# Optimization experiments

Measured on AMD Instinct MI355X. Metric: run time of the kernel, lower is better.

Reference implementation:

```python
import jax, jax.numpy as jnp
import numpy as np

HIDDEN_DIM = 1024
SEQ_LEN = 4096
D_IN = 1024


def setup_inputs() -> dict:
    key = jax.random.key(0)
    ks = jax.random.split(key, 9)
    s = 1.0 / np.sqrt(D_IN)
    return {
        "q": jax.random.normal(ks[0], (SEQ_LEN, D_IN), jnp.float32),
        "k": jax.random.normal(ks[1], (SEQ_LEN, D_IN), jnp.float32),
        "v": jax.random.normal(ks[2], (SEQ_LEN, D_IN), jnp.float32),
        "Wq": jax.random.normal(ks[3], (D_IN, HIDDEN_DIM), jnp.float32) * s,
        "bq": jnp.zeros((HIDDEN_DIM,), jnp.float32),
        "Wk": jax.random.normal(ks[4], (D_IN, HIDDEN_DIM), jnp.float32) * s,
        "bk": jnp.zeros((HIDDEN_DIM,), jnp.float32),
        "Wv": jax.random.normal(ks[5], (D_IN, HIDDEN_DIM), jnp.float32) * s,
        "bv": jnpp_zeros() if False else jnp.zeros((HIDDEN_DIM,), jnp.float32),
    }


def reference(q, k, v, Wq, bq, Wk, bk, Wv, bv):
    # Dense projections (flax Dense: x @ W + b)
    query = q @ Wq + bq          # [S, H]
    key_p = k @ Wk + bk          # [S, H]
    value = v @ Wv + bv          # [S, H]
    # scores = Q K^T / sqrt(hidden_dim)  -> [S, S]
    scores = jnp.matmul(query, key_p.T) / jnp.sqrt(jnp.float32(HIDDEN_DIM))
    weights = jax.nn.softmax(scores, axis=-1)
    context = jnp.matmul(weights, value)  # [S, H]
    return context
```

## Files before the change

### kernel.cpp

```cpp
#include <hip/hip_runtime.h>


typedef short short4v __attribute__((ext_vector_type(4)));
typedef short short8  __attribute__((ext_vector_type(8)));
typedef float f32x4   __attribute__((ext_vector_type(4)));

#define MFMA16 __builtin_amdgcn_mfma_f32_16x16x32_bf16

__device__ __forceinline__ short f2bf(float f) {
    union { float f; unsigned u; } x; x.f = f;
    unsigned r = (x.u + 0x7FFFu + ((x.u >> 16) & 1u)) >> 16;
    return (short)r;
}
__device__ __forceinline__ float bf2f(short s) {
    union { unsigned u; float f; } x;
    x.u = ((unsigned)(unsigned short)s) << 16; return x.f;
}
__device__ __forceinline__ void store_out(short* p, float v) { *p = f2bf(v); }
__device__ __forceinline__ void store_out(float* p, float v) { *p = v; }

__device__ __forceinline__ void gl2lds(const short* g, short* l) {
    __builtin_amdgcn_global_load_lds(
        (const __attribute__((address_space(1))) void*)g,
        (__attribute__((address_space(3))) void*)l, 16, 0, 0);
}

__global__ __launch_bounds__(256) void prep_w(
    const float* __restrict__ W0, const float* __restrict__ W1,
    const float* __restrict__ W2, short* __restrict__ Wt)
{
    __shared__ float tile[64][65];
    const float* W = blockIdx.z == 0 ? W0 : (blockIdx.z == 1 ? W1 : W2);
    short* T = Wt + (size_t)blockIdx.z * 1048576;
    const int c0 = blockIdx.x * 64;
    const int r0 = blockIdx.y * 64;
    const int tx = threadIdx.x & 63;
    const int ty = threadIdx.x >> 6;
    #pragma unroll
    for (int p = 0; p < 16; ++p) {
        int r = ty + p * 4;
        tile[r][tx] = W[(size_t)(r0 + r) * 1024 + c0 + tx];
    }
    __syncthreads();
    #pragma unroll
    for (int p = 0; p < 16; ++p) {
        int r = ty + p * 4;
        T[(size_t)(c0 + r) * 1024 + r0 + tx] = f2bf(tile[tx][r]);
    }
}

__global__ __launch_bounds__(256) void cast_qkv(
    const float* __restrict__ q, const float* __restrict__ k,
    const float* __restrict__ v, short* __restrict__ xb)
{
    const float* src = blockIdx.z == 0 ? q : (blockIdx.z == 1 ? k : v);
    short* dst = xb + (size_t)blockIdx.z * 4194304;
    for (int i = blockIdx.x * 256 + threadIdx.x; i < 1048576; i += 256 * 1024) {
        float4 f = ((const float4*)src)[i];
        short4v o;
        o[0] = f2bf(f.x); o[1] = f2bf(f.y); o[2] = f2bf(f.z); o[3] = f2bf(f.w);
        ((short4v*)dst)[i] = o;
    }
}

template <typename TOut, int MODE>
__global__ __launch_bounds__(256) void gemm64(
    const short* __restrict__ A, const short* __restrict__ Bt,
    const float* __restrict__ b0, const float* __restrict__ b1,
    const float* __restrict__ b2, TOut* __restrict__ C,
    short* __restrict__ Vt,
    int M, int N, int Kd, int lda, int ldb, float scale, int kiters)
{
    constexpr int LDSN = (MODE == 1) ? (128 * 136) : (128 * 64 * 2);
    __shared__ short Lds[LDSN];
    short* As = Lds;
    short* Bs = Lds + 128 * 64;

    const int t    = threadIdx.x;
    const int lane = t & 63;
    const int wv   = t >> 6;

    const int nb  = gridDim.x;
    const int bid = blockIdx.y * nb + blockIdx.x;
    const int band   = bid / (8 * nb);
    const int within = bid - band * 8 * nb;
    const int m0 = (band * 8 + (within & 7)) * 128;
    const int n0 = (within >> 3) * 128;

    const float* bias = nullptr;
    int kbeg = 0;
    if constexpr (MODE == 1) {
        const int z = blockIdx.z;
        A  += (size_t)z * M * lda;
        Bt += (size_t)z * N * ldb;
        C  += (size_t)z * M * N;
        bias = z == 0 ? b0 : (z == 1 ? b1 : b2);
    }
    if constexpr (MODE == 2) {
        kbeg = blockIdx.z * kiters * 64;
        C += (size_t)blockIdx.z * M * N;
    }
    (void)b0; (void)b1; (void)b2;

    const int sr = lane >> 3;
    const int sc = (lane & 7) ^ sr;
    const short* pA = A  + (size_t)(m0 + wv * 32 + sr) * lda + kbeg + sc * 8;
    const short* pB = Bt + (size_t)(n0 + wv * 32 + sr) * ldb + kbeg + sc * 8;
    const size_t a8 = (size_t)8 * lda;
    const size_t b8 = (size_t)8 * ldb;
    short* lA = As + wv * 2048;
    short* lB = Bs + wv * 2048;

    const int wm = wv & 1, wn = wv >> 1;
    const int lr = lane & 15, lq = lane >> 4;
    const int xkey = lr & 7;

    f32x4 acc[4][4];
    #pragma unroll
    for (int i = 0; i < 4; ++i)
        #pragma unroll
        for (int j = 0; j < 4; ++j) {
            f32x4 z = {0.f, 0.f, 0.f, 0.f};
            acc[i][j] = z;
        }

    for (int kk = 0; kk < kiters; ++kk) {
        #pragma unroll
        for (int r = 0; r < 4; ++r) gl2lds(pA + r * a8, lA + r * 512);
        #pragma unroll
        for (int r = 0; r < 4; ++r) gl2lds(pB + r * b8, lB + r * 512);
        pA += 64; pB += 64;
        __syncthreads();

        #pragma unroll
        for (int h = 0; h < 2; ++h) {
            short8 af[4], bfr[4];
            #pragma unroll
            for (int i = 0; i < 4; ++i)
                af[i] = *(const short8*)
                    &As[(wm * 64 + i * 16 + lr) * 64 + (((h * 4 + lq) ^ xkey) * 8)];
            #pragma unroll
            for (int j = 0; j < 4; ++j)
                bfr[j] = *(const short8*)
                    &Bs[(wn * 64 + j * 16 + lr) * 64 + (((h * 4 + lq) ^ xkey) * 8)];
            #pragma unroll
            for (int i = 0; i < 4; ++i)
                #pragma unroll
                for (int j = 0; j < 4; ++j)
                    acc[i][j] = MFMA16(af[i], bfr[j], acc[i][j], 0, 0, 0);
        }
        __syncthreads();
    }

    if constexpr (MODE == 1) {
        if (blockIdx.z == 2) {
            #pragma unroll
            for (int i = 0; i < 4; ++i) {
                #pragma unroll
                for (int j = 0; j < 4; ++j) {
                    const int colL = wn * 64 + j * 16 + lr;
                    const float bb = bias[n0 + colL];
                    #pragma unroll
                    for (int r = 0; r < 4; ++r) {
                        const int rowL = wm * 64 + i * 16 + lq * 4 + r;
                        Lds[colL * 136 + rowL] = f2bf(acc[i][j][r] * scale + bb);
                    }
                }
            }
            __syncthreads();
            const int c = t >> 1, part = t & 1;
            short* dst = Vt + (size_t)(n0 + c) * 4096 + m0 + part * 64;
            #pragma unroll
            for (int s = 0; s < 8; ++s)
                *(short8*)(dst + s * 8) =
                    *(const short8*)&Lds[c * 136 + part * 64 + s * 8];
            return;
        }
    }
    #pragma unroll
    for (int i = 0; i < 4; ++i) {
        #pragma unroll
        for (int j = 0; j < 4; ++j) {
            const int crow = m0 + wm * 64 + i * 16 + lq * 4;
            const int ccol = n0 + wn * 64 + j * 16 + lr;
            float bb = 0.f;
            if constexpr (MODE == 1) bb = bias[ccol];
            #pragma unroll
            for (int r = 0; r < 4; ++r) {
                float val = acc[i][j][r] * scale + bb;
                store_out(&C[(size_t)(crow + r) * N + ccol], val);
            }
        }
    }
}

__global__ __launch_bounds__(256) void softmax_bf16(short* __restrict__ S)
{
    const int row = blockIdx.x;
    short8* r8 = (short8*)(S + (size_t)row * 4096);
    const int t = threadIdx.x;

    float x[16];
    #pragma unroll
    for (int i = 0; i < 2; ++i) {
        short8 raw = r8[t + 256 * i];
        #pragma unroll
        for (int j = 0; j < 8; ++j) x[8 * i + j] = bf2f(raw[j]);
    }
    float m = -1e30f;
    #pragma unroll
    for (int i = 0; i < 16; ++i) m = fmaxf(m, x[i]);
    #pragma unroll
    for (int off = 32; off > 0; off >>= 1) m = fmaxf(m, __shfl_xor(m, off));

    __shared__ float redm[4], reds[4];
    const int wv = t >> 6;
    if ((t & 63) == 0) redm[wv] = m;
    __syncthreads();
    m = fmaxf(fmaxf(redm[0], redm[1]), fmaxf(redm[2], redm[3]));

    float s = 0.f;
    #pragma unroll
    for (int i = 0; i < 16; ++i) { x[i] = __expf(x[i] - m); s += x[i]; }
    #pragma unroll
    for (int off = 32; off > 0; off >>= 1) s += __shfl_xor(s, off);
    if ((t & 63) == 0) reds[wv] = s;
    __syncthreads();
    s = reds[0] + reds[1] + reds[2] + reds[3];
    const float inv = 1.f / s;

    #pragma unroll
    for (int i = 0; i < 2; ++i) {
        short8 o;
        #pragma unroll
        for (int j = 0; j < 8; ++j) o[j] = f2bf(x[8 * i + j] * inv);
        r8[t + 256 * i] = o;
    }
}

__global__ __launch_bounds__(256) void combine(
    const float* __restrict__ p0, const float* __restrict__ p1,
    float* __restrict__ out)
{
    for (int i = blockIdx.x * 256 + threadIdx.x; i < 1048576; i += 256 * 1024) {
        float4 a = ((const float4*)p0)[i];
        float4 b = ((const float4*)p1)[i];
        float4 o; o.x = a.x + b.x; o.y = a.y + b.y;
        o.z = a.z + b.z; o.w = a.w + b.w;
        ((float4*)out)[i] = o;
    }
}

extern "C" void kernel_launch(void* const* d_in, const int* in_sizes, int n_in,
                              void* d_out, int out_size, void* d_ws, size_t ws_size,
                              hipStream_t stream)
{
    const float* q  = (const float*)d_in[0];
    const float* k  = (const float*)d_in[1];
    const float* v  = (const float*)d_in[2];
    const float* Wq = (const float*)d_in[3];
    const float* bq = (const float*)d_in[4];
    const float* Wk = (const float*)d_in[5];
    const float* bk = (const float*)d_in[6];
    const float* Wv = (const float*)d_in[7];
    const float* bv = (const float*)d_in[8];
    float* out = (float*)d_out;

    char* ws = (char*)d_ws;
    const size_t MB = 1ull << 20;
    short* Wt = (short*)(ws + 0);
    short* xb = (short*)(ws + 6 * MB);
    short* pr = (short*)(ws + 30 * MB);
    short* Vt = (short*)(ws + 46 * MB);
    short* S  = (short*)(ws + 54 * MB);
    float* p0 = (float*)(ws + 0);
    float* p1 = p0 + 4194304;

    prep_w<<<dim3(16, 16, 3), 256, 0, stream>>>(Wq, Wk, Wv, Wt);
    cast_qkv<<<dim3(1024, 1, 3), 256, 0, stream>>>(q, k, v, xb);
    gemm64<short, 1><<<dim3(8, 32, 3), 256, 0, stream>>>(
        xb, Wt, bq, bk, bv, pr, Vt, 4096, 1024, 1024, 1024, 1024, 1.f, 16);
    gemm64<short, 0><<<dim3(32, 32), 256, 0, stream>>>(
        pr, pr + 4194304, nullptr, nullptr, nullptr, S, nullptr,
        4096, 4096, 1024, 1024, 1024, 0.03125f, 16);
    softmax_bf16<<<4096, 256, 0, stream>>>(S);
    gemm64<float, 2><<<dim3(8, 32, 2), 256, 0, stream>>>(
        S, Vt, nullptr, nullptr, nullptr, p0, nullptr,
        4096, 1024, 4096, 4096, 4096, 1.f, 32);
    combine<<<1024, 256, 0, stream>>>(p0, p1, out);
}
```

Before: 269.4 us.

## Replace 128x128 GEMM with 256x256 tile, 4-stage pipelined LDS GEMM and split-K

Replaces the 128x128, 256-thread GEMM kernel with a 256x256, 512-thread kernel. It runs a 4-deep global-to-LDS prefetch ring with explicit vmcnt waits and barriers, and raises wave priority around the MFMA blocks. The V transpose moves out of the projection epilogue into a separate transpose kernel. The final P·V GEMM uses 3- or 4-way split-K, chosen by workspace size, and the partials are summed in a generalized combine. The aim is more data reuse per tile and hiding global load latency behind MFMA work. In exchange, fewer blocks are launched, register pressure rises, and an extra transpose pass is added.

```diff
diff --git a/kernel.cpp b/kernel.cpp
--- a/kernel.cpp
+++ b/kernel.cpp
@@ -63,132 +63,153 @@
     }
 }
 
+__global__ __launch_bounds__(256) void transpose_v(
+    const short* __restrict__ src, short* __restrict__ dst)
+{
+    __shared__ short t[64][65];
+    const int c0 = blockIdx.x * 64;
+    const int r0 = blockIdx.y * 64;
+    const int tx = threadIdx.x & 63;
+    const int ty = threadIdx.x >> 6;
+    #pragma unroll
+    for (int p = 0; p < 16; ++p) {
+        const int r = p * 4 + ty;
+        t[r][tx] = src[(size_t)(r0 + r) * 1024 + c0 + tx];
+    }
+    __syncthreads();
+    #pragma unroll
+    for (int p = 0; p < 16; ++p) {
+        const int r = p * 4 + ty;
+        dst[(size_t)(c0 + r) * 4096 + r0 + tx] = t[tx][r];
+    }
+}
+
 template <typename TOut, int MODE>
-__global__ __launch_bounds__(256) void gemm64(
+__global__ __launch_bounds__(512, 2) void gemm256(
     const short* __restrict__ A, const short* __restrict__ Bt,
     const float* __restrict__ b0, const float* __restrict__ b1,
-    const float* __restrict__ b2, TOut* __restrict__ C,
-    short* __restrict__ Vt,
-    int M, int N, int Kd, int lda, int ldb, float scale, int kiters)
-{
-    constexpr int LDSN = (MODE == 1) ? (128 * 136) : (128 * 64 * 2);
-    __shared__ short Lds[LDSN];
-    short* As = Lds;
-    short* Bs = Lds + 128 * 64;
+    const float* __restrict__ b2,
+    TOut* __restrict__ C, float* __restrict__ P1, float* __restrict__ P2,
+    float* __restrict__ P3,
+    int M, int N, int lda, int ldb, float scale,
+    int nc, int nc_last, int kstep)
+{
+    __shared__ short Lds[65536];
 
     const int t    = threadIdx.x;
     const int lane = t & 63;
     const int wv   = t >> 6;
 
-    const int nb  = gridDim.x;
-    const int bid = blockIdx.y * nb + blockIdx.x;
-    const int band   = bid / (8 * nb);
-    const int within = bid - band * 8 * nb;
-    const int m0 = (band * 8 + (within & 7)) * 128;
-    const int n0 = (within >> 3) * 128;
+    int m0, n0;
+    {
+        const int nb  = gridDim.x;
+        const int bid = blockIdx.y * nb + blockIdx.x;
+        if (nb == 16 && gridDim.y == 16) {
+            const int x = bid & 7, i = bid >> 3;
+            m0 = ((x & 1) * 8 + (i & 7)) * 256;
+            n0 = ((x >> 1) * 4 + (i >> 3)) * 256;
+        } else {
+            const int band   = bid / (8 * nb);
+            const int within = bid - band * 8 * nb;
+            m0 = (band * 8 + (within & 7)) * 256;
+            n0 = (within >> 3) * 256;
+        }
+    }
 
     const float* bias = nullptr;
     int kbeg = 0;
+    TOut* Cw = C;
     if constexpr (MODE == 1) {
         const int z = blockIdx.z;
         A  += (size_t)z * M * lda;
         Bt += (size_t)z * N * ldb;
-        C  += (size_t)z * M * N;
+        Cw  = C + (size_t)z * M * N;
         bias = z == 0 ? b0 : (z == 1 ? b1 : b2);
     }
     if constexpr (MODE == 2) {
-        kbeg = blockIdx.z * kiters * 64;
-        C += (size_t)blockIdx.z * M * N;
-    }
-    (void)b0; (void)b1; (void)b2;
-
-    const int sr = lane >> 3;
-    const int sc = (lane & 7) ^ sr;
-    const short* pA = A  + (size_t)(m0 + wv * 32 + sr) * lda + kbeg + sc * 8;
-    const short* pB = Bt + (size_t)(n0 + wv * 32 + sr) * ldb + kbeg + sc * 8;
-    const size_t a8 = (size_t)8 * lda;
-    const size_t b8 = (size_t)8 * ldb;
-    short* lA = As + wv * 2048;
-    short* lB = Bs + wv * 2048;
-
-    const int wm = wv & 1, wn = wv >> 1;
+        const int z = blockIdx.z;
+        kbeg = z * kstep;
+        if (z == (int)gridDim.z - 1) nc = nc_last;
+        Cw = (TOut*)(z == 0 ? (float*)C : (z == 1 ? P1 : (z == 2 ? P2 : P3)));
+    }
+    (void)b0; (void)b1; (void)b2; (void)P1; (void)P2; (void)P3;
+    (void)nc_last; (void)kstep;
+
+    const int srow = lane >> 2;
+    const int skof = (lane & 3) * 8;
+    const short* pA0 = A  + (size_t)(m0 + wv * 16 + srow) * lda + kbeg + skof;
+    const short* pA1 = pA0 + (size_t)128 * lda;
+    const short* pB0 = Bt + (size_t)(n0 + wv * 16 + srow) * ldb + kbeg + skof;
+    const short* pB1 = pB0 + (size_t)128 * ldb;
+    short* sA0 = Lds + wv * 512;
+    short* sA1 = Lds + 4096  + wv * 512;
+    short* sB0 = Lds + 8192  + wv * 512;
+    short* sB1 = Lds + 12288 + wv * 512;
+
+    const int wm = wv >> 2, wn = wv & 3;
     const int lr = lane & 15, lq = lane >> 4;
-    const int xkey = lr & 7;
-
-    f32x4 acc[4][4];
-    #pragma unroll
-    for (int i = 0; i < 4; ++i)
+    const short* rdA = Lds + (wm * 128 + lr) * 32 + lq * 8;
+    const short* rdB = Lds + 8192 + (wn * 64 + lr) * 32 + lq * 8;
+
+    f32x4 acc[8][4];
+    #pragma unroll
+    for (int i = 0; i < 8; ++i)
+        #pragma unroll
+        for (int j = 0; j < 4; ++j) { f32x4 z4 = {0.f,0.f,0.f,0.f}; acc[i][j] = z4; }
+
+#define STAGE(c) {                                                        \
+    const int su_ = (c) & 3;                                              \
+    const size_t ko_ = (size_t)(c) * 32;                                  \
+    gl2lds(pA0 + ko_, sA0 + su_ * 16384);                                 \
+    gl2lds(pA1 + ko_, sA1 + su_ * 16384);                                 \
+    gl2lds(pB0 + ko_, sB0 + su_ * 16384);                                 \
+    gl2lds(pB1 + ko_, sB1 + su_ * 16384); }
+
+    STAGE(0); STAGE(1); STAGE(2);
+    asm volatile("s_waitcnt vmcnt(8)" ::: "memory");
+    __builtin_amdgcn_s_barrier();
+
+#define PHASE(c, DOSTAGE, VMN) {                                          \
+    const int u_ = (c) & 3;                                               \
+    const short* rA_ = rdA + u_ * 16384;                                  \
+    const short* rB_ = rdB + u_ * 16384;                                  \
+    short8 af[8], bfr[4];                                                 \
+    _Pragma("unroll") for (int i = 0; i < 8; ++i)                         \
+        af[i] = *(const short8*)(rA_ + i * 512);                          \
+    _Pragma("unroll") for (int j = 0; j < 4; ++j)                         \
+        bfr[j] = *(const short8*)(rB_ + j * 512);                         \
+    if (DOSTAGE) STAGE((c) + 3);                                          \
+    __builtin_amdgcn_s_barrier();                                         \
+    __builtin_amdgcn_s_setprio(1);                                        \
+    _Pragma("unroll") for (int i = 0; i < 8; ++i)                         \
+        _Pragma("unroll") for (int j = 0; j < 4; ++j)                     \
+            acc[i][j] = MFMA16(af[i], bfr[j], acc[i][j], 0, 0, 0);        \
+    __builtin_amdgcn_s_setprio(0);                                        \
+    if ((VMN) == 8)      asm volatile("s_waitcnt vmcnt(8)" ::: "memory"); \
+    else if ((VMN) == 4) asm volatile("s_waitcnt vmcnt(4)" ::: "memory"); \
+    else if ((VMN) == 0) asm volatile("s_waitcnt vmcnt(0)" ::: "memory"); \
+    if ((VMN) >= 0) __builtin_amdgcn_s_barrier(); }
+
+    #pragma unroll 4
+    for (int c = 0; c < nc - 3; ++c) PHASE(c, 1, 8);
+    PHASE(nc - 3, 0, 4);
+    PHASE(nc - 2, 0, 0);
+    PHASE(nc - 1, 0, -1);
+#undef PHASE
+#undef STAGE
+
+    #pragma unroll
+    for (int i = 0; i < 8; ++i) {
+        const int crow = m0 + wm * 128 + i * 16 + lq * 4;
         #pragma unroll
         for (int j = 0; j < 4; ++j) {
-            f32x4 z = {0.f, 0.f, 0.f, 0.f};
-            acc[i][j] = z;
-        }
-
-    for (int kk = 0; kk < kiters; ++kk) {
-        #pragma unroll
-        for (int r = 0; r < 4; ++r) gl2lds(pA + r * a8, lA + r * 512);
-        #pragma unroll
-        for (int r = 0; r < 4; ++r) gl2lds(pB + r * b8, lB + r * 512);
-        pA += 64; pB += 64;
-        __syncthreads();
-
-        #pragma unroll
-        for (int h = 0; h < 2; ++h) {
-            short8 af[4], bfr[4];
-            #pragma unroll
-            for (int i = 0; i < 4; ++i)
-                af[i] = *(const short8*)
-                    &As[(wm * 64 + i * 16 + lr) * 64 + (((h * 4 + lq) ^ xkey) * 8)];
-            #pragma unroll
-            for (int j = 0; j < 4; ++j)
-                bfr[j] = *(const short8*)
-                    &Bs[(wn * 64 + j * 16 + lr) * 64 + (((h * 4 + lq) ^ xkey) * 8)];
-            #pragma unroll
-            for (int i = 0; i < 4; ++i)
-                #pragma unroll
-                for (int j = 0; j < 4; ++j)
-                    acc[i][j] = MFMA16(af[i], bfr[j], acc[i][j], 0, 0, 0);
-        }
-        __syncthreads();
-    }
-
-    if constexpr (MODE == 1) {
-        if (blockIdx.z == 2) {
-            #pragma unroll
-            for (int i = 0; i < 4; ++i) {
-                #pragma unroll
-                for (int j = 0; j < 4; ++j) {
-                    const int colL = wn * 64 + j * 16 + lr;
-                    const float bb = bias[n0 + colL];
-                    #pragma unroll
-                    for (int r = 0; r < 4; ++r) {
-                        const int rowL = wm * 64 + i * 16 + lq * 4 + r;
-                        Lds[colL * 136 + rowL] = f2bf(acc[i][j][r] * scale + bb);
-                    }
-                }
-            }
-            __syncthreads();
-            const int c = t >> 1, part = t & 1;
-            short* dst = Vt + (size_t)(n0 + c) * 4096 + m0 + part * 64;
-            #pragma unroll
-            for (int s = 0; s < 8; ++s)
-                *(short8*)(dst + s * 8) =
-                    *(const short8*)&Lds[c * 136 + part * 64 + s * 8];
-            return;
-        }
-    }
-    #pragma unroll
-    for (int i = 0; i < 4; ++i) {
-        #pragma unroll
-        for (int j = 0; j < 4; ++j) {
-            const int crow = m0 + wm * 64 + i * 16 + lq * 4;
             const int ccol = n0 + wn * 64 + j * 16 + lr;
             float bb = 0.f;
             if constexpr (MODE == 1) bb = bias[ccol];
             #pragma unroll
             for (int r = 0; r < 4; ++r) {
                 float val = acc[i][j][r] * scale + bb;
-                store_out(&C[(size_t)(crow + r) * N + ccol], val);
+                store_out(&Cw[(size_t)(crow + r) * N + ccol], val);
             }
         }
     }
@@ -239,14 +260,19 @@
 }
 
 __global__ __launch_bounds__(256) void combine(
-    const float* __restrict__ p0, const float* __restrict__ p1,
-    float* __restrict__ out)
+    float* __restrict__ out, const float* __restrict__ a,
+    const float* __restrict__ b, const float* __restrict__ c, int np)
 {
     for (int i = blockIdx.x * 256 + threadIdx.x; i < 1048576; i += 256 * 1024) {
-        float4 a = ((const float4*)p0)[i];
-        float4 b = ((const float4*)p1)[i];
-        float4 o; o.x = a.x + b.x; o.y = a.y + b.y;
-        o.z = a.z + b.z; o.w = a.w + b.w;
+        float4 o = ((const float4*)out)[i];
+        float4 x = ((const float4*)a)[i];
+        float4 y = ((const float4*)b)[i];
+        o.x += x.x + y.x; o.y += x.y + y.y;
+        o.z += x.z + y.z; o.w += x.w + y.w;
+        if (np == 3) {
+            float4 w = ((const float4*)c)[i];
+            o.x += w.x; o.y += w.y; o.z += w.z; o.w += w.w;
+        }
         ((float4*)out)[i] = o;
     }
 }
@@ -271,21 +297,33 @@
     short* Wt = (short*)(ws + 0);
     short* xb = (short*)(ws + 6 * MB);
     short* pr = (short*)(ws + 30 * MB);
-    short* Vt = (short*)(ws + 46 * MB);
-    short* S  = (short*)(ws + 54 * MB);
-    float* p0 = (float*)(ws + 0);
-    float* p1 = p0 + 4194304;
+    short* S  = (short*)(ws + 46 * MB);
+    short* Vt = (short*)(ws + 78 * MB);
+    float* p1 = (float*)(ws + 0);
+    float* p2 = (float*)(ws + 16 * MB);
+    float* p3 = (float*)(ws + 86 * MB);
+    const int SK = (ws_size >= 102 * MB) ? 4 : 3;
 
     prep_w<<<dim3(16, 16, 3), 256, 0, stream>>>(Wq, Wk, Wv, Wt);
     cast_qkv<<<dim3(1024, 1, 3), 256, 0, stream>>>(q, k, v, xb);
-    gemm64<short, 1><<<dim3(8, 32, 3), 256, 0, stream>>>(
-        xb, Wt, bq, bk, bv, pr, Vt, 4096, 1024, 1024, 1024, 1024, 1.f, 16);
-    gemm64<short, 0><<<dim3(32, 32), 256, 0, stream>>>(
-        pr, pr + 4194304, nullptr, nullptr, nullptr, S, nullptr,
-        4096, 4096, 1024, 1024, 1024, 0.03125f, 16);
+    gemm256<short, 1><<<dim3(4, 16, 3), 512, 0, stream>>>(
+        xb, Wt, bq, bk, bv, pr, nullptr, nullptr, nullptr,
+        4096, 1024, 1024, 1024, 1.f, 32, 32, 0);
+    transpose_v<<<dim3(16, 64), 256, 0, stream>>>(pr + 8 * 1024 * 1024, Vt);
+    gemm256<short, 0><<<dim3(16, 16), 512, 0, stream>>>(
+        pr, pr + 4 * 1024 * 1024, nullptr, nullptr, nullptr, S,
+        nullptr, nullptr, nullptr,
+        4096, 4096, 1024, 1024, 0.03125f, 32, 32, 0);
     softmax_bf16<<<4096, 256, 0, stream>>>(S);
-    gemm64<float, 2><<<dim3(8, 32, 2), 256, 0, stream>>>(
-        S, Vt, nullptr, nullptr, nullptr, p0, nullptr,
-        4096, 1024, 4096, 4096, 4096, 1.f, 32);
-    combine<<<1024, 256, 0, stream>>>(p0, p1, out);
-}
+    if (SK == 4) {
+        gemm256<float, 2><<<dim3(4, 16, 4), 512, 0, stream>>>(
+            S, Vt, nullptr, nullptr, nullptr, out, p1, p2, p3,
+            4096, 1024, 4096, 4096, 1.f, 32, 32, 1024);
+        combine<<<1024, 256, 0, stream>>>(out, p1, p2, p3, 3);
+    } else {
+        gemm256<float, 2><<<dim3(4, 16, 3), 512, 0, stream>>>(
+            S, Vt, nullptr, nullptr, nullptr, out, p1, p2, nullptr,
+            4096, 1024, 4096, 4096, 1.f, 42, 44, 1344);
+        combine<<<1024, 256, 0, stream>>>(out, p1, p2, nullptr, 2);
+    }
+}
```

Measured after the change: 259.6 us. 3.7% less time.
